# Performance work log

Hardware: AMD Instinct MI355X
Metric: run time of the kernel (lower is better)

## Reference

```python
import jax, jax.numpy as jnp
import numpy as np

# dims
B, S, E, H, W = 32, 256, 512, 512, 512   # batch, max_sentence_length, word_emb, rnn_units, weight_size
ENC = 2 * H                               # bidirectional encoder hidden
V = 50000                                 # vocab


def setup_inputs() -> dict:
    key = jax.random.key(0)
    ks = jax.random.split(key, 16)
    n = jax.random.normal
    return {
        "word_ids": jax.random.randint(ks[0], (B, S), 0, V),
        "encoder_outputs": n(ks[1], (B, S, ENC), jnp.float32),
        "encoder_hn": n(ks[2], (B, H), jnp.float32),          # initial decoder cell state
        "emb": n(ks[3], (V, E), jnp.float32) * 0.02,          # WordFeature embedding table
        "chunk_emb": n(ks[4], (S, W), jnp.float32) * 0.02,    # chunk_length_embedding
        "W1": n(ks[5], (ENC, W), jnp.float32) / np.sqrt(ENC),
        "W2": n(ks[6], (E, W), jnp.float32) / np.sqrt(E),
        "W3": n(ks[7], (E, W), jnp.float32) / np.sqrt(E),
        "W4": n(ks[8], (H, W), jnp.float32) / np.sqrt(H),
        "vt1": n(ks[9], (W,), jnp.float32) / np.sqrt(W),
        "vt2": n(ks[10], (W,), jnp.float32) / np.sqrt(W),
        "Wx": n(ks[11], (E, 4 * H), jnp.float32) / np.sqrt(E),  # decoder LSTM cell
        "Wh": n(ks[12], (H, 4 * H), jnp.float32) / np.sqrt(H),
        "bias": jnp.zeros((4 * H,), jnp.float32),
    }


def reference(word_ids, encoder_outputs, encoder_hn, emb, chunk_emb,
              W1, W2, W3, W4, vt1, vt2, Wx, Wh, bias):
    Ss = word_ids.shape[1]
    Hh = encoder_hn.shape[1]
    inp = emb[word_ids]                                   # [B,S,E] word features
    b1 = jnp.einsum('bse,ew->bsw', encoder_outputs, W1)   # W1(encoder_output), hoisted
    b2 = jnp.einsum('bse,ew->bsw', inp, W2)               # W2(single_input), hoisted
    pos = jnp.arange(Ss)

    def decode_one(inp_b, b1_b, b2_b, c0):
        def step(carry, _):
            last_bond, bond, h, c, out_vec = carry
            done = bond >= Ss
            # decoder input: mean of current segment inp[last_bond:bond] (zeros at step 0)
            m = ((pos >= last_bond) & (pos < bond)).astype(inp_b.dtype)  # [S]
            x = (m @ inp_b) / jnp.maximum(m.sum(), 1.0)                  # [E]
            # LSTM cell (stand-in for decoder.pointer_forward)
            gates = x @ Wx + h @ Wh + bias                               # [4H]
            i_g, f_g, g_g, o_g = jnp.split(gates, 4)
            c_n = jax.nn.sigmoid(f_g) * c + jax.nn.sigmoid(i_g) * jnp.tanh(g_g)
            h_n = jax.nn.sigmoid(o_g) * jnp.tanh(c_n)
            h2 = jnp.where(done, h, h_n)
            c2 = jnp.where(done, c, c_n)
            bidx = jnp.minimum(bond, Ss - 1)
            # pointer attention over positions >= bond
            blend = jnp.tanh(b1_b + b2_b + inp_b[bidx] @ W3 + h2 @ W4)   # [S,W]
            seg_len = jnp.clip(bond - last_bond, 0, Ss - 1)
            scores = blend @ vt1 + chunk_emb[seg_len] @ vt2              # [S]
            scores = jnp.where(pos >= bidx, scores, -1e30)
            # log_softmax is monotonic -> argmax of scores == argmax of log-probs
            idx = jnp.argmax(scores)                                     # absolute = max_index + bond
            new_bond = jnp.where(idx > bond, idx, bond + 1)              # force progress
            widx = jnp.minimum(new_bond, Ss - 1)
            val = jnp.where((~done) & (new_bond < Ss), 1.0, out_vec[widx])
            out_new = out_vec.at[widx].set(val)
            last2 = jnp.where(done, last_bond, bond)
            bond2 = jnp.where(done, bond, new_bond)
            return (last2, bond2, h2, c2, out_new), None

        init = (jnp.int32(0), jnp.int32(0),
                jnp.zeros((Hh,), inp_b.dtype), c0,
                jnp.zeros((Ss,), inp_b.dtype))
        (_, _, _, _, out_vec), _ = jax.lax.scan(step, init, None, length=Ss)
        return out_vec

    outs = jax.vmap(decode_one)(inp, b1, b2, encoder_hn)   # [B,S]
    return outs.T                                          # [S,B] == torch.stack(output_list, 1)
```

## Files before the change

kernel.cpp:

```cpp
#include <hip/hip_runtime.h>
#include <math.h>

#define Bn   32
#define Sn   256
#define En   512
#define Hn   512
#define Wn   512
#define ENCn 1024
#define G4   2048
#define KTOT 1536

#define OFF_BSUM  0L
#define OFF_U3    4194304L
#define OFF_PE    8388608L
#define OFF_WB    12599296L
#define OFF_W4B   14696448L
#define OFF_GATES 14958592L
#define OFF_H     15089664L
#define OFF_C     15106048L
#define OFF_SPART 15138816L
#define OFF_STATE 15204352L

typedef unsigned long long u64t;

__device__ __forceinline__ float aload(const float* p) {
    return __hip_atomic_load(p, __ATOMIC_RELAXED, __HIP_MEMORY_SCOPE_AGENT);
}
__device__ __forceinline__ void astore(float* p, float v) {
    __hip_atomic_store(p, v, __ATOMIC_RELAXED, __HIP_MEMORY_SCOPE_AGENT);
}
__device__ __forceinline__ int aiload(const int* p) {
    return __hip_atomic_load(p, __ATOMIC_RELAXED, __HIP_MEMORY_SCOPE_AGENT);
}
__device__ __forceinline__ void aistore(int* p, int v) {
    __hip_atomic_store(p, v, __ATOMIC_RELAXED, __HIP_MEMORY_SCOPE_AGENT);
}
__device__ __forceinline__ u64t aload64(const u64t* p) {
    return __hip_atomic_load(p, __ATOMIC_RELAXED, __HIP_MEMORY_SCOPE_AGENT);
}
__device__ __forceinline__ void astore64(u64t* p, u64t v) {
    __hip_atomic_store(p, v, __ATOMIC_RELAXED, __HIP_MEMORY_SCOPE_AGENT);
}
__device__ __forceinline__ u64t pack2(float a, float b) {
    return (u64t)__float_as_uint(a) | ((u64t)__float_as_uint(b) << 32);
}
__device__ __forceinline__ float lo32(u64t v) { return __uint_as_float((unsigned)(v & 0xffffffffu)); }
__device__ __forceinline__ float hi32(u64t v) { return __uint_as_float((unsigned)(v >> 32)); }

__global__ void init_kernel(const float* __restrict__ hn0, float* __restrict__ h,
                            float* __restrict__ c, int* __restrict__ state)
{
    int i = blockIdx.x * blockDim.x + threadIdx.x;
    if (i < Bn * Hn) { h[i] = 0.0f; c[i] = hn0[i]; }
    if (i < 8192) state[i] = 0;
}

__global__ void wtrans_kernel(const float* __restrict__ Wx, const float* __restrict__ Wh,
                              const float* __restrict__ W4, float* __restrict__ WB,
                              float* __restrict__ W4B)
{
    int idx = blockIdx.x * 256 + threadIdx.x;
    if (idx < 2097152) {
        const int cc = idx & 3, l = (idx >> 2) & 63, kq = (idx >> 8) & 255, cb = idx >> 16;
        const int k = 4 * kq + cc, j = cb * 64 + l;
        WB[idx] = (k < 512) ? Wx[(long)k * G4 + j] : Wh[(long)(k - 512) * G4 + j];
    }
    if (idx < 262144) {
        const int cc = idx & 3, l = (idx >> 2) & 63, kq = (idx >> 8) & 127, cb = idx >> 15;
        const int k = 4 * kq + cc, j = cb * 64 + l;
        W4B[idx] = W4[(long)k * Wn + j];
    }
}

__global__ void pe1_kernel(const int* __restrict__ wid, const float* __restrict__ emb,
                           float* __restrict__ pb)
{
    const int b = blockIdx.x, blk = blockIdx.y;
    __shared__ int wids[16];
    if (threadIdx.x < 16) wids[threadIdx.x] = wid[b * Sn + blk * 16 + threadIdx.x];
    __syncthreads();
    float a0 = 0.f, a1 = 0.f;
    for (int s = 0; s < 16; ++s) {
        const float* r = emb + (long)wids[s] * En;
        a0 += r[threadIdx.x]; a1 += r[threadIdx.x + 256];
    }
    pb[((long)b * 16 + blk) * En + threadIdx.x] = a0;
    pb[((long)b * 16 + blk) * En + threadIdx.x + 256] = a1;
}

__global__ void pe2_kernel(const int* __restrict__ wid, const float* __restrict__ emb,
                           const float* __restrict__ pb, float* __restrict__ pe)
{
    const int b = blockIdx.x, blk = blockIdx.y;
    __shared__ int wids[16];
    if (threadIdx.x < 16) wids[threadIdx.x] = wid[b * Sn + blk * 16 + threadIdx.x];
    __syncthreads();
    float a0 = 0.f, a1 = 0.f;
    for (int j = 0; j < blk; ++j) {
        a0 += pb[((long)b * 16 + j) * En + threadIdx.x];
        a1 += pb[((long)b * 16 + j) * En + threadIdx.x + 256];
    }
    float* base = pe + (long)b * 257 * En;
    if (blk == 0) { base[threadIdx.x] = 0.f; base[threadIdx.x + 256] = 0.f; }
    for (int s = 0; s < 16; ++s) {
        const float* r = emb + (long)wids[s] * En;
        a0 += r[threadIdx.x]; a1 += r[threadIdx.x + 256];
        float* o = base + (long)(blk * 16 + s + 1) * En;
        o[threadIdx.x] = a0; o[threadIdx.x + 256] = a1;
    }
}

__global__ __launch_bounds__(256) void bsum_gemm(
    const float* __restrict__ enc, const int* __restrict__ wid,
    const float* __restrict__ emb, const float* __restrict__ W1,
    const float* __restrict__ W2, float* __restrict__ bsum)
{
    __shared__ float As[16][68];
    __shared__ float Bs[16][68];
    const int tid  = threadIdx.x;
    const int row0 = blockIdx.y * 64;
    const int col0 = blockIdx.x * 64;
    const int tm0  = (tid & 15) * 4;
    const int tn0  = (tid >> 4) * 4;
    const int la_r = tid >> 2;
    const int la_k = (tid & 3) * 4;
    const int lb_k = tid >> 4;
    const int lb_n = (tid & 15) * 4;

    float acc[4][4];
#pragma unroll
    for (int i = 0; i < 4; i++)
#pragma unroll
        for (int j = 0; j < 4; j++) acc[i][j] = 0.0f;

    for (int k0 = 0; k0 < KTOT; k0 += 16) {
        const int gr = row0 + la_r;
        float4 av;
        if (k0 < ENCn) {
            av = *(const float4*)&enc[(long)gr * ENCn + k0 + la_k];
        } else {
            const int wv = wid[gr];
            av = *(const float4*)&emb[(long)wv * En + (k0 - ENCn) + la_k];
        }
        As[la_k + 0][la_r] = av.x;
        As[la_k + 1][la_r] = av.y;
        As[la_k + 2][la_r] = av.z;
        As[la_k + 3][la_r] = av.w;
        float4 bv;
        if (k0 < ENCn) bv = *(const float4*)&W1[(long)(k0 + lb_k) * Wn + col0 + lb_n];
        else           bv = *(const float4*)&W2[(long)(k0 - ENCn + lb_k) * Wn + col0 + lb_n];
        *(float4*)&Bs[lb_k][lb_n] = bv;
        __syncthreads();
#pragma unroll
        for (int kk = 0; kk < 16; kk++) {
            float4 a = *(const float4*)&As[kk][tm0];
            float4 b = *(const float4*)&Bs[kk][tn0];
            acc[0][0] += a.x * b.x; acc[0][1] += a.x * b.y; acc[0][2] += a.x * b.z; acc[0][3] += a.x * b.w;
            acc[1][0] += a.y * b.x; acc[1][1] += a.y * b.y; acc[1][2] += a.y * b.z; acc[1][3] += a.y * b.w;
            acc[2][0] += a.z * b.x; acc[2][1] += a.z * b.y; acc[2][2] += a.z * b.z; acc[2][3] += a.z * b.w;
            acc[3][0] += a.w * b.x; acc[3][1] += a.w * b.y; acc[3][2] += a.w * b.z; acc[3][3] += a.w * b.w;
        }
        __syncthreads();
    }
#pragma unroll
    for (int i = 0; i < 4; i++) {
        float4 o = make_float4(acc[i][0], acc[i][1], acc[i][2], acc[i][3]);
        *(float4*)&bsum[(long)(row0 + tm0 + i) * Wn + col0 + tn0] = o;
    }
}

__global__ __launch_bounds__(256) void u3_gemm(
    const int* __restrict__ wid, const float* __restrict__ emb,
    const float* __restrict__ W3, float* __restrict__ u3)
{
    __shared__ float As[16][68];
    __shared__ float Bs[16][68];
    const int tid  = threadIdx.x;
    const int row0 = blockIdx.y * 64;
    const int col0 = blockIdx.x * 64;
    const int tm0  = (tid & 15) * 4;
    const int tn0  = (tid >> 4) * 4;
    const int la_r = tid >> 2;
    const int la_k = (tid & 3) * 4;
    const int lb_k = tid >> 4;
    const int lb_n = (tid & 15) * 4;

    float acc[4][4];
#pragma unroll
    for (int i = 0; i < 4; i++)
#pragma unroll
        for (int j = 0; j < 4; j++) acc[i][j] = 0.0f;

    for (int k0 = 0; k0 < 512; k0 += 16) {
        const int gr = row0 + la_r;
        const int wv = wid[gr];
        float4 av = *(const float4*)&emb[(long)wv * En + k0 + la_k];
        As[la_k + 0][la_r] = av.x;
        As[la_k + 1][la_r] = av.y;
        As[la_k + 2][la_r] = av.z;
        As[la_k + 3][la_r] = av.w;
        *(float4*)&Bs[lb_k][lb_n] = *(const float4*)&W3[(long)(k0 + lb_k) * Wn + col0 + lb_n];
        __syncthreads();
#pragma unroll
        for (int kk = 0; kk < 16; kk++) {
            float4 a = *(const float4*)&As[kk][tm0];
            float4 b = *(const float4*)&Bs[kk][tn0];
            acc[0][0] += a.x * b.x; acc[0][1] += a.x * b.y; acc[0][2] += a.x * b.z; acc[0][3] += a.x * b.w;
            acc[1][0] += a.y * b.x; acc[1][1] += a.y * b.y; acc[1][2] += a.y * b.z; acc[1][3] += a.y * b.w;
            acc[2][0] += a.z * b.x; acc[2][1] += a.z * b.y; acc[2][2] += a.z * b.z; acc[2][3] += a.z * b.w;
            acc[3][0] += a.w * b.x; acc[3][1] += a.w * b.y; acc[3][2] += a.w * b.z; acc[3][3] += a.w * b.w;
        }
        __syncthreads();
    }
#pragma unroll
    for (int i = 0; i < 4; i++) {
        float4 o = make_float4(acc[i][0], acc[i][1], acc[i][2], acc[i][3]);
        *(float4*)&u3[(long)(row0 + tm0 + i) * Wn + col0 + tn0] = o;
    }
}

__global__ __launch_bounds__(256) void decode_kernel(
    const float* __restrict__ bias, const float* __restrict__ vt1,
    const float* __restrict__ bsum, const float* __restrict__ u3,
    const float* __restrict__ pe,   const float* __restrict__ WB,
    const float* __restrict__ W4B,  float* __restrict__ gpart,
    float* __restrict__ hbuf, float* __restrict__ cbuf,
    float* __restrict__ spart,
    int* __restrict__ state, float* __restrict__ out)
{
    __shared__ __align__(16) float wlds[32768];
    __shared__ __align__(16) float sx[4096];
    __shared__ __align__(16) float sred[2048];
    __shared__ float s_svt[64];
    __shared__ float s_wv[4];
    __shared__ int   s_wi[4];
    __shared__ int   s_bd[8], s_ls[8];
    __shared__ int   s_exit;

    const int wg   = blockIdx.x;
    const int tid  = threadIdx.x;
    const int lane = tid & 63;
    const int wv   = tid >> 6;

    u64t* s64   = (u64t*)state;
    int*  garr  = state + 2560;
    int*  sflag = state + 4608;

    const int cb1 = wg & 31;
    const int kh  = (wg >> 5) & 1;
    const int bg  = wg >> 6;
    const int b2  = wg >> 3;
    const int cb2 = wg & 7;
    const int bq2 = (wg >> 3) & 7;
    const float4* W4B4 = (const float4*)W4B;
    float4* wlds4 = (float4*)wlds;
    float4* sx4   = (float4*)sx;
    u64t* gp64 = (u64t*)gpart;
    u64t* h64  = (u64t*)hbuf;
    u64t* c64  = (u64t*)cbuf;
    const float2* pef2  = (const float2*)pe;
    const float2* bias2 = (const float2*)bias;

    {
        const float4* src = (const float4*)WB + ((long)cb1 * 256 + kh * 128) * 64;
        for (int i = tid; i < 8192; i += 256) wlds4[i] = src[i];
    }
    if (tid < 64) s_svt[tid] = vt1[cb2 * 64 + tid];

    int a_b = 0;

    for (int t = 1; t <= Sn; ++t) {
        if (tid < 64) {
            const bool isb = tid < 8;
            const u64t* sp = s64 + 768 + 16 * (bg * 8 + (tid & 7));
            for (;;) {
                const u64t pk = isb ? aload64(sp) : 0ULL;
                const int ep = (int)(pk & 0xffffu);
                const int bd = (int)((pk >> 16) & 0xffffu);
                const bool ok = !isb || (ep >= t - 1) || (bd >= Sn);
                const bool dn = isb && (bd >= Sn);
                const u64t okb = __ballot(ok);
                const u64t dnb = __ballot(dn);
                if ((okb & 0xffULL) == 0xffULL) {
                    if (isb) { s_bd[tid] = bd; s_ls[tid] = (int)((pk >> 32) & 0xffffu); }
                    if (tid == 0) s_exit = ((dnb & 0xffULL) == 0xffULL);
                    break;
                }
                __builtin_amdgcn_s_sleep(1);
            }
        }
        __syncthreads();
        if (s_exit) break;

        for (int idx = tid; idx < 2048; idx += 256) {
            const int bq = idx >> 8, kp = idx & 255;
            const int b  = bg * 8 + bq;
            float v0 = 0.f, v1 = 0.f;
            if (s_bd[bq] < Sn) {
                if (kh == 0) {
                    const int bd = s_bd[bq], ls = s_ls[bq];
                    const float inv = 1.0f / (float)max(bd - ls, 1);
                    const float2 pa = pef2[((long)b * 257 + bd) * 256 + kp];
                    const float2 pb_ = pef2[((long)b * 257 + ls) * 256 + kp];
                    v0 = (pa.x - pb_.x) * inv;
                    v1 = (pa.y - pb_.y) * inv;
                } else {
                    const u64t hv = aload64(&h64[b * 256 + kp]);
                    v0 = lo32(hv); v1 = hi32(hv);
                }
            }
            sx[bq * 512 + 2 * kp]     = v0;
            sx[bq * 512 + 2 * kp + 1] = v1;
        }
        __syncthreads();
        {
            float acc[8] = {0.f,0.f,0.f,0.f,0.f,0.f,0.f,0.f};
            const float4* wl = wlds4 + (wv * 32) * 64 + lane;
#pragma unroll 8
            for (int kq = 0; kq < 32; ++kq) {
                const float4 w = wl[kq * 64];
                const int kb = wv * 32 + kq;
#pragma unroll
                for (int bq = 0; bq < 8; ++bq) {
                    const float4 xv = sx4[bq * 128 + kb];
                    acc[bq] += w.x * xv.x + w.y * xv.y + w.z * xv.z + w.w * xv.w;
                }
            }
#pragma unroll
            for (int bq = 0; bq < 8; ++bq)
                sred[wv * 512 + bq * 64 + lane] = acc[bq];
        }
        __syncthreads();
        {
            const int bq = tid >> 5, cp = tid & 31;
            if (s_bd[bq] < Sn) {
                const int c0 = 2 * cp, c1 = 2 * cp + 1;
                const float lo = sred[bq * 64 + c0] + sred[512 + bq * 64 + c0]
                               + sred[1024 + bq * 64 + c0] + sred[1536 + bq * 64 + c0];
                const float hi = sred[bq * 64 + c1] + sred[512 + bq * 64 + c1]
                               + sred[1024 + bq * 64 + c1] + sred[1536 + bq * 64 + c1];
                astore64(&gp64[(long)(kh * Bn + bg * 8 + bq) * 1024 + cb1 * 32 + cp], pack2(lo, hi));
            }
        }
        __syncthreads();
        if (tid < 8)
            aistore(&garr[64 * (bg * 8 + tid) + cb1 * 2 + kh], t);

        const int bd = s_bd[bq2];
        if (bd < Sn) {
            ++a_b;
            if (tid < 64) {
                while (aiload(&garr[64 * b2 + tid]) < t) __builtin_amdgcn_s_sleep(1);
            }
            __syncthreads();
            {
                const long base0 = (long)b2 * 1024;
                const long base1 = (long)(Bn + b2) * 1024;
                const u64t gi0 = aload64(&gp64[base0 + 0 * 256 + tid]);
                const u64t gf0 = aload64(&gp64[base0 + 1 * 256 + tid]);
                const u64t gg0 = aload64(&gp64[base0 + 2 * 256 + tid]);
                const u64t go0 = aload64(&gp64[base0 + 3 * 256 + tid]);
                const u64t gi1 = aload64(&gp64[base1 + 0 * 256 + tid]);
                const u64t gf1 = aload64(&gp64[base1 + 1 * 256 + tid]);
                const u64t gg1 = aload64(&gp64[base1 + 2 * 256 + tid]);
                const u64t go1 = aload64(&gp64[base1 + 3 * 256 + tid]);
                const u64t cv  = aload64(&c64[((a_b - 1) & 1) * 8192 + b2 * 256 + tid]);
                const float2 bi = bias2[0 * 256 + tid];
                const float2 bf = bias2[1 * 256 + tid];
                const float2 bg_ = bias2[2 * 256 + tid];
                const float2 bo = bias2[3 * 256 + tid];
                float h2a, h2b, cna, cnb;
                {
                    const float ig = lo32(gi0) + lo32(gi1) + bi.x;
                    const float fg = lo32(gf0) + lo32(gf1) + bf.x;
                    const float gg = lo32(gg0) + lo32(gg1) + bg_.x;
                    const float og = lo32(go0) + lo32(go1) + bo.x;
                    const float sf = 1.f / (1.f + expf(-fg));
                    const float si = 1.f / (1.f + expf(-ig));
                    const float so = 1.f / (1.f + expf(-og));
                    cna = sf * lo32(cv) + si * tanhf(gg);
                    h2a = so * tanhf(cna);
                }
                {
                    const float ig = hi32(gi0) + hi32(gi1) + bi.y;
                    const float fg = hi32(gf0) + hi32(gf1) + bf.y;
                    const float gg = hi32(gg0) + hi32(gg1) + bg_.y;
                    const float og = hi32(go0) + hi32(go1) + bo.y;
                    const float sf = 1.f / (1.f + expf(-fg));
                    const float si = 1.f / (1.f + expf(-ig));
                    const float so = 1.f / (1.f + expf(-og));
                    cnb = sf * hi32(cv) + si * tanhf(gg);
                    h2b = so * tanhf(cnb);
                }
                sx[2 * tid]     = h2a;
                sx[2 * tid + 1] = h2b;
                if (cb2 == 0) {
                    astore64(&h64[b2 * 256 + tid], pack2(h2a, h2b));
                    astore64(&c64[(a_b & 1) * 8192 + b2 * 256 + tid], pack2(cna, cnb));
                }
            }
            __syncthreads();
            {
                float acc = 0.f;
                const float4* wrow = W4B4 + ((long)cb2 * 128 + wv * 32) * 64 + lane;
#pragma unroll 8
                for (int kq = 0; kq < 32; ++kq) {
                    const float4 w  = wrow[(long)kq * 64];
                    const float4 xv = sx4[wv * 32 + kq];
                    acc += w.x * xv.x + w.y * xv.y + w.z * xv.z + w.w * xv.w;
                }
                sx[512 + wv * 64 + lane] = acc;
            }
            __syncthreads();
            if (tid < 64) {
                const float* u3row = u3 + ((long)b2 * Sn + bd) * Wn + cb2 * 64;
                sx[768 + tid] = sx[512 + tid] + sx[576 + tid] + sx[640 + tid]
                              + sx[704 + tid] + u3row[tid];
            }
            __syncthreads();
            if (tid >= bd) {
                const float* row = bsum + ((long)b2 * Sn + tid) * Wn + cb2 * 64;
                float a = 0.f;
#pragma unroll 8
                for (int i = 0; i < 64; ++i)
                    a += tanhf(row[i] + sx[768 + i]) * s_svt[i];
                astore(&spart[((long)b2 * 8 + cb2) * 256 + tid], a);
            }
            __syncthreads();
            if (cb2 != 0) {
                if (tid == 0) aistore(&sflag[16 * b2 + cb2], a_b);
            } else {
                if (tid >= 1 && tid < 8) {
                    while (aiload(&sflag[16 * b2 + tid]) < a_b) __builtin_amdgcn_s_sleep(1);
                }
                __syncthreads();
                float v = -3.402823e38f; int vi = Sn;
                if (tid >= bd) {
                    const float* sp = spart + (long)b2 * 8 * 256 + tid;
                    float s = 0.f;
#pragma unroll
                    for (int k = 0; k < 8; ++k) s += aload(&sp[k * 256]);
                    v = s; vi = tid;
                }
#pragma unroll
                for (int off = 32; off; off >>= 1) {
                    const float v2 = __shfl_xor(v, off, 64);
                    const int   i2 = __shfl_xor(vi, off, 64);
                    if (v2 > v || (v2 == v && i2 < vi)) { v = v2; vi = i2; }
                }
                if (lane == 0) { s_wv[wv] = v; s_wi[wv] = vi; }
                __syncthreads();
                if (tid == 0) {
                    float bv = s_wv[0]; int bi_ = s_wi[0];
#pragma unroll
                    for (int k = 1; k < 4; ++k)
                        if (s_wv[k] > bv || (s_wv[k] == bv && s_wi[k] < bi_)) { bv = s_wv[k]; bi_ = s_wi[k]; }
                    const int nb2 = (bi_ > bd) ? bi_ : bd + 1;
                    if (nb2 < Sn) out[nb2 * Bn + b2] = 1.0f;
                    const u64t pk =
                        (u64t)(unsigned)t |
                        ((u64t)(unsigned)nb2 << 16) |
                        ((u64t)(unsigned)bd  << 32);
                    astore64(&s64[768 + 16 * b2], pk);
                }
            }
        }
    }
}

extern "C" void kernel_launch(void* const* d_in, const int* in_sizes, int n_in,
                              void* d_out, int out_size, void* d_ws, size_t ws_size,
                              hipStream_t stream)
{
    const int*   wid  = (const int*)d_in[0];
    const float* enc  = (const float*)d_in[1];
    const float* hn0  = (const float*)d_in[2];
    const float* emb  = (const float*)d_in[3];
    const float* W1   = (const float*)d_in[5];
    const float* W2   = (const float*)d_in[6];
    const float* W3   = (const float*)d_in[7];
    const float* W4   = (const float*)d_in[8];
    const float* vt1  = (const float*)d_in[9];
    const float* Wx   = (const float*)d_in[11];
    const float* Wh   = (const float*)d_in[12];
    const float* bias = (const float*)d_in[13];

    float* ws    = (float*)d_ws;
    float* bsum  = ws + OFF_BSUM;
    float* u3    = ws + OFF_U3;
    float* pb    = ws + OFF_U3;
    float* pe    = ws + OFF_PE;
    float* WB    = ws + OFF_WB;
    float* W4B   = ws + OFF_W4B;
    float* gpart = ws + OFF_GATES;
    float* h     = ws + OFF_H;
    float* c     = ws + OFF_C;
    float* spart = ws + OFF_SPART;
    int*   state = (int*)(ws + OFF_STATE);
    float* out   = (float*)d_out;

    hipMemsetAsync(d_out, 0, (size_t)Sn * Bn * sizeof(float), stream);
    hipLaunchKernelGGL(init_kernel, dim3(64), dim3(256), 0, stream, hn0, h, c, state);
    hipLaunchKernelGGL(wtrans_kernel, dim3(8192), dim3(256), 0, stream, Wx, Wh, W4, WB, W4B);
    hipLaunchKernelGGL(pe1_kernel, dim3(32, 16), dim3(256), 0, stream, wid, emb, pb);
    hipLaunchKernelGGL(pe2_kernel, dim3(32, 16), dim3(256), 0, stream, wid, emb, pb, pe);
    hipLaunchKernelGGL(u3_gemm, dim3(8, 128), dim3(256), 0, stream, wid, emb, W3, u3);
    hipLaunchKernelGGL(bsum_gemm, dim3(8, 128), dim3(256), 0, stream, enc, wid, emb, W1, W2, bsum);

    void* args[] = { (void*)&bias, (void*)&vt1, (void*)&bsum, (void*)&u3, (void*)&pe,
                     (void*)&WB, (void*)&W4B, (void*)&gpart, (void*)&h, (void*)&c,
                     (void*)&spart, (void*)&state, (void*)&out };
    hipLaunchCooperativeKernel((void*)decode_kernel, dim3(256), dim3(256), args, 0, stream);
}
```

Baseline: 800.5 us.

## Decouple x and h gate phases with separate flags and redundant per-block argmax

Splits the gate partial buffers into an input part and a double-buffered hidden part. Blocks computing the h-side product now wait only on a per-batch h-ready flag, while x-side blocks wait on the bond state, which loosens the coupling between the two halves. The cross-block argmax reduction is now done redundantly by all eight score blocks, so each keeps its own bond locally instead of waiting on a single leader block. The u3 row is prefetched before the gate wait. In exchange the protocol gains more flags and parity-indexed buffers, which raises the risk of ordering races.

```diff
diff --git a/kernel.cpp b/kernel.cpp
--- a/kernel.cpp
+++ b/kernel.cpp
@@ -9,17 +9,19 @@
 #define ENCn 1024
 #define G4   2048
 #define KTOT 1536
+#define BIGF 0x40000000
 
 #define OFF_BSUM  0L
 #define OFF_U3    4194304L
 #define OFF_PE    8388608L
 #define OFF_WB    12599296L
 #define OFF_W4B   14696448L
-#define OFF_GATES 14958592L
-#define OFF_H     15089664L
-#define OFF_C     15106048L
-#define OFF_SPART 15138816L
-#define OFF_STATE 15204352L
+#define OFF_GPX   14958592L
+#define OFF_GPH   15024128L
+#define OFF_H     15155200L
+#define OFF_C     15171584L
+#define OFF_SPART 15204352L
+#define OFF_STATE 15335424L
 
 typedef unsigned long long u64t;
 
@@ -223,7 +225,8 @@
     const float* __restrict__ bias, const float* __restrict__ vt1,
     const float* __restrict__ bsum, const float* __restrict__ u3,
     const float* __restrict__ pe,   const float* __restrict__ WB,
-    const float* __restrict__ W4B,  float* __restrict__ gpart,
+    const float* __restrict__ W4B,  float* __restrict__ gpx,
+    float* __restrict__ gph,
     float* __restrict__ hbuf, float* __restrict__ cbuf,
     float* __restrict__ spart,
     int* __restrict__ state, float* __restrict__ out)
@@ -235,29 +238,30 @@
     __shared__ float s_wv[4];
     __shared__ int   s_wi[4];
     __shared__ int   s_bd[8], s_ls[8];
-    __shared__ int   s_exit;
+    __shared__ int   s_p1done;
 
     const int wg   = blockIdx.x;
     const int tid  = threadIdx.x;
     const int lane = tid & 63;
     const int wv   = tid >> 6;
 
-    u64t* s64   = (u64t*)state;
-    int*  garr  = state + 2560;
-    int*  sflag = state + 4608;
+    u64t* s64g  = (u64t*)state;
+    int*  hflag = state + 1024;
+    int*  garr  = state + 2048;
+    int*  sflag = state + 4096;
 
     const int cb1 = wg & 31;
     const int kh  = (wg >> 5) & 1;
     const int bg  = wg >> 6;
     const int b2  = wg >> 3;
     const int cb2 = wg & 7;
-    const int bq2 = (wg >> 3) & 7;
     const float4* W4B4 = (const float4*)W4B;
     float4* wlds4 = (float4*)wlds;
     float4* sx4   = (float4*)sx;
-    u64t* gp64 = (u64t*)gpart;
-    u64t* h64  = (u64t*)hbuf;
-    u64t* c64  = (u64t*)cbuf;
+    u64t* gpx64 = (u64t*)gpx;
+    u64t* gph64 = (u64t*)gph;
+    u64t* h64   = (u64t*)hbuf;
+    u64t* c64   = (u64t*)cbuf;
     const float2* pef2  = (const float2*)pe;
     const float2* bias2 = (const float2*)bias;
 
@@ -267,108 +271,137 @@
     }
     if (tid < 64) s_svt[tid] = vt1[cb2 * 64 + tid];
 
-    int a_b = 0;
+    bool p1done = false, p2done = false;
+    int my_bd = 0, my_ls = 0;
 
     for (int t = 1; t <= Sn; ++t) {
-        if (tid < 64) {
-            const bool isb = tid < 8;
-            const u64t* sp = s64 + 768 + 16 * (bg * 8 + (tid & 7));
-            for (;;) {
-                const u64t pk = isb ? aload64(sp) : 0ULL;
-                const int ep = (int)(pk & 0xffffu);
-                const int bd = (int)((pk >> 16) & 0xffffu);
-                const bool ok = !isb || (ep >= t - 1) || (bd >= Sn);
-                const bool dn = isb && (bd >= Sn);
-                const u64t okb = __ballot(ok);
-                const u64t dnb = __ballot(dn);
-                if ((okb & 0xffULL) == 0xffULL) {
-                    if (isb) { s_bd[tid] = bd; s_ls[tid] = (int)((pk >> 32) & 0xffffu); }
-                    if (tid == 0) s_exit = ((dnb & 0xffULL) == 0xffULL);
-                    break;
-                }
-                __builtin_amdgcn_s_sleep(1);
+        if (p1done && p2done) break;
+
+        if (!p1done) {
+            if (kh == 0) {
+                if (tid < 64) {
+                    const bool isb = tid < 8;
+                    const u64t* sp = s64g + 8 * (bg * 8 + (tid & 7));
+                    for (;;) {
+                        const u64t pk = isb ? aload64(sp) : 0ULL;
+                        const int ep = (int)(pk & 0xffffu);
+                        const int bd = (int)((pk >> 16) & 0xffffu);
+                        const bool ok = !isb || (ep >= t - 1) || (bd >= Sn);
+                        const u64t okb = __ballot(ok);
+                        const u64t dnb = __ballot(isb && (bd >= Sn));
+                        if ((okb & 0xffULL) == 0xffULL) {
+                            if (isb) { s_bd[tid] = bd; s_ls[tid] = (int)((pk >> 32) & 0xffffu); }
+                            if (tid == 0) s_p1done = ((dnb & 0xffULL) == 0xffULL);
+                            break;
+                        }
+                        __builtin_amdgcn_s_sleep(1);
+                    }
+                }
+            } else {
+                if (tid < 64) {
+                    const bool isb = tid < 8;
+                    const int* hp = hflag + 16 * (bg * 8 + (tid & 7));
+                    for (;;) {
+                        const int hf = isb ? aiload(hp) : 0x7ffffff0;
+                        const bool ok = (hf >= t - 1);
+                        const u64t okb = __ballot(ok);
+                        const u64t dnb = __ballot(isb && (hf >= BIGF));
+                        if ((okb & 0xffULL) == 0xffULL) {
+                            if (isb) { s_bd[tid] = (hf >= BIGF) ? Sn : 0; s_ls[tid] = 0; }
+                            if (tid == 0) s_p1done = ((dnb & 0xffULL) == 0xffULL);
+                            break;
+                        }
+                        __builtin_amdgcn_s_sleep(1);
+                    }
+                }
+            }
+            __syncthreads();
+            if (s_p1done) p1done = true;
+            if (!p1done) {
+                for (int idx = tid; idx < 2048; idx += 256) {
+                    const int bq = idx >> 8, kp = idx & 255;
+                    const int b  = bg * 8 + bq;
+                    float v0 = 0.f, v1 = 0.f;
+                    if (s_bd[bq] < Sn) {
+                        if (kh == 0) {
+                            const int bd = s_bd[bq], ls = s_ls[bq];
+                            const float inv = 1.0f / (float)max(bd - ls, 1);
+                            const float2 pa  = pef2[((long)b * 257 + bd) * 256 + kp];
+                            const float2 pb_ = pef2[((long)b * 257 + ls) * 256 + kp];
+                            v0 = (pa.x - pb_.x) * inv;
+                            v1 = (pa.y - pb_.y) * inv;
+                        } else {
+                            const u64t hv = aload64(&h64[b * 256 + kp]);
+                            v0 = lo32(hv); v1 = hi32(hv);
+                        }
+                    }
+                    sx[bq * 512 + 2 * kp]     = v0;
+                    sx[bq * 512 + 2 * kp + 1] = v1;
+                }
+                __syncthreads();
+                {
+                    float acc[8] = {0.f,0.f,0.f,0.f,0.f,0.f,0.f,0.f};
+                    const float4* wl = wlds4 + (wv * 32) * 64 + lane;
+#pragma unroll 8
+                    for (int kq = 0; kq < 32; ++kq) {
+                        const float4 w = wl[kq * 64];
+                        const int kb = wv * 32 + kq;
+#pragma unroll
+                        for (int bq = 0; bq < 8; ++bq) {
+                            const float4 xv = sx4[bq * 128 + kb];
+                            acc[bq] += w.x * xv.x + w.y * xv.y + w.z * xv.z + w.w * xv.w;
+                        }
+                    }
+#pragma unroll
+                    for (int bq = 0; bq < 8; ++bq)
+                        sred[wv * 512 + bq * 64 + lane] = acc[bq];
+                }
+                __syncthreads();
+                {
+                    const int bq = tid >> 5, cp = tid & 31;
+                    if (s_bd[bq] < Sn) {
+                        const int c0 = 2 * cp, c1 = 2 * cp + 1;
+                        const float lo = sred[bq * 64 + c0] + sred[512 + bq * 64 + c0]
+                                       + sred[1024 + bq * 64 + c0] + sred[1536 + bq * 64 + c0];
+                        const float hi = sred[bq * 64 + c1] + sred[512 + bq * 64 + c1]
+                                       + sred[1024 + bq * 64 + c1] + sred[1536 + bq * 64 + c1];
+                        if (kh == 0)
+                            astore64(&gpx64[(long)(bg * 8 + bq) * 1024 + cb1 * 32 + cp], pack2(lo, hi));
+                        else
+                            astore64(&gph64[(long)(t & 1) * 32768 + (long)(bg * 8 + bq) * 1024 + cb1 * 32 + cp], pack2(lo, hi));
+                    }
+                }
+                __syncthreads();
+                if (tid < 8)
+                    aistore(&garr[64 * (bg * 8 + tid) + cb1 * 2 + kh], t);
             }
         }
-        __syncthreads();
-        if (s_exit) break;
-
-        for (int idx = tid; idx < 2048; idx += 256) {
-            const int bq = idx >> 8, kp = idx & 255;
-            const int b  = bg * 8 + bq;
-            float v0 = 0.f, v1 = 0.f;
-            if (s_bd[bq] < Sn) {
-                if (kh == 0) {
-                    const int bd = s_bd[bq], ls = s_ls[bq];
-                    const float inv = 1.0f / (float)max(bd - ls, 1);
-                    const float2 pa = pef2[((long)b * 257 + bd) * 256 + kp];
-                    const float2 pb_ = pef2[((long)b * 257 + ls) * 256 + kp];
-                    v0 = (pa.x - pb_.x) * inv;
-                    v1 = (pa.y - pb_.y) * inv;
-                } else {
-                    const u64t hv = aload64(&h64[b * 256 + kp]);
-                    v0 = lo32(hv); v1 = hi32(hv);
-                }
-            }
-            sx[bq * 512 + 2 * kp]     = v0;
-            sx[bq * 512 + 2 * kp + 1] = v1;
-        }
-        __syncthreads();
-        {
-            float acc[8] = {0.f,0.f,0.f,0.f,0.f,0.f,0.f,0.f};
-            const float4* wl = wlds4 + (wv * 32) * 64 + lane;
-#pragma unroll 8
-            for (int kq = 0; kq < 32; ++kq) {
-                const float4 w = wl[kq * 64];
-                const int kb = wv * 32 + kq;
-#pragma unroll
-                for (int bq = 0; bq < 8; ++bq) {
-                    const float4 xv = sx4[bq * 128 + kb];
-                    acc[bq] += w.x * xv.x + w.y * xv.y + w.z * xv.z + w.w * xv.w;
-                }
-            }
-#pragma unroll
-            for (int bq = 0; bq < 8; ++bq)
-                sred[wv * 512 + bq * 64 + lane] = acc[bq];
-        }
-        __syncthreads();
-        {
-            const int bq = tid >> 5, cp = tid & 31;
-            if (s_bd[bq] < Sn) {
-                const int c0 = 2 * cp, c1 = 2 * cp + 1;
-                const float lo = sred[bq * 64 + c0] + sred[512 + bq * 64 + c0]
-                               + sred[1024 + bq * 64 + c0] + sred[1536 + bq * 64 + c0];
-                const float hi = sred[bq * 64 + c1] + sred[512 + bq * 64 + c1]
-                               + sred[1024 + bq * 64 + c1] + sred[1536 + bq * 64 + c1];
-                astore64(&gp64[(long)(kh * Bn + bg * 8 + bq) * 1024 + cb1 * 32 + cp], pack2(lo, hi));
-            }
-        }
-        __syncthreads();
-        if (tid < 8)
-            aistore(&garr[64 * (bg * 8 + tid) + cb1 * 2 + kh], t);
-
-        const int bd = s_bd[bq2];
-        if (bd < Sn) {
-            ++a_b;
+
+        if (!p2done) {
+            const int bd = my_bd;
+            float u3v = 0.f;
+            if (tid < 64) u3v = aload(&u3[((long)b2 * Sn + bd) * Wn + cb2 * 64 + tid]);
             if (tid < 64) {
-                while (aiload(&garr[64 * b2 + tid]) < t) __builtin_amdgcn_s_sleep(1);
+                const int* gp = garr + 64 * b2 + tid;
+                while (aiload(gp) < t) __builtin_amdgcn_s_sleep(1);
             }
             __syncthreads();
             {
-                const long base0 = (long)b2 * 1024;
-                const long base1 = (long)(Bn + b2) * 1024;
-                const u64t gi0 = aload64(&gp64[base0 + 0 * 256 + tid]);
-                const u64t gf0 = aload64(&gp64[base0 + 1 * 256 + tid]);
-                const u64t gg0 = aload64(&gp64[base0 + 2 * 256 + tid]);
-                const u64t go0 = aload64(&gp64[base0 + 3 * 256 + tid]);
-                const u64t gi1 = aload64(&gp64[base1 + 0 * 256 + tid]);
-                const u64t gf1 = aload64(&gp64[base1 + 1 * 256 + tid]);
-                const u64t gg1 = aload64(&gp64[base1 + 2 * 256 + tid]);
-                const u64t go1 = aload64(&gp64[base1 + 3 * 256 + tid]);
-                const u64t cv  = aload64(&c64[((a_b - 1) & 1) * 8192 + b2 * 256 + tid]);
-                const float2 bi = bias2[0 * 256 + tid];
-                const float2 bf = bias2[1 * 256 + tid];
+                const long bx = (long)b2 * 1024;
+                const long bh = (long)(t & 1) * 32768 + (long)b2 * 1024;
+                const u64t gi0 = aload64(&gpx64[bx + 0 * 256 + tid]);
+                const u64t gf0 = aload64(&gpx64[bx + 1 * 256 + tid]);
+                const u64t gg0 = aload64(&gpx64[bx + 2 * 256 + tid]);
+                const u64t go0 = aload64(&gpx64[bx + 3 * 256 + tid]);
+                const u64t gi1 = aload64(&gph64[bh + 0 * 256 + tid]);
+                const u64t gf1 = aload64(&gph64[bh + 1 * 256 + tid]);
+                const u64t gg1 = aload64(&gph64[bh + 2 * 256 + tid]);
+                const u64t go1 = aload64(&gph64[bh + 3 * 256 + tid]);
+                const u64t cv  = aload64(&c64[(long)((t - 1) & 1) * 8192 + b2 * 256 + tid]);
+                const float2 bi  = bias2[0 * 256 + tid];
+                const float2 bf  = bias2[1 * 256 + tid];
                 const float2 bg_ = bias2[2 * 256 + tid];
-                const float2 bo = bias2[3 * 256 + tid];
+                const float2 bo  = bias2[3 * 256 + tid];
                 float h2a, h2b, cna, cnb;
                 {
                     const float ig = lo32(gi0) + lo32(gi1) + bi.x;
@@ -396,10 +429,11 @@
                 sx[2 * tid + 1] = h2b;
                 if (cb2 == 0) {
                     astore64(&h64[b2 * 256 + tid], pack2(h2a, h2b));
-                    astore64(&c64[(a_b & 1) * 8192 + b2 * 256 + tid], pack2(cna, cnb));
-                }
-            }
-            __syncthreads();
+                    astore64(&c64[(long)(t & 1) * 8192 + b2 * 256 + tid], pack2(cna, cnb));
+                }
+            }
+            __syncthreads();
+            if (cb2 == 0 && tid == 0) aistore(&hflag[16 * b2], t);
             {
                 float acc = 0.f;
                 const float4* wrow = W4B4 + ((long)cb2 * 128 + wv * 32) * 64 + lane;
@@ -413,9 +447,8 @@
             }
             __syncthreads();
             if (tid < 64) {
-                const float* u3row = u3 + ((long)b2 * Sn + bd) * Wn + cb2 * 64;
                 sx[768 + tid] = sx[512 + tid] + sx[576 + tid] + sx[640 + tid]
-                              + sx[704 + tid] + u3row[tid];
+                              + sx[704 + tid] + u3v;
             }
             __syncthreads();
             if (tid >= bd) {
@@ -424,46 +457,49 @@
 #pragma unroll 8
                 for (int i = 0; i < 64; ++i)
                     a += tanhf(row[i] + sx[768 + i]) * s_svt[i];
-                astore(&spart[((long)b2 * 8 + cb2) * 256 + tid], a);
-            }
-            __syncthreads();
-            if (cb2 != 0) {
-                if (tid == 0) aistore(&sflag[16 * b2 + cb2], a_b);
-            } else {
-                if (tid >= 1 && tid < 8) {
-                    while (aiload(&sflag[16 * b2 + tid]) < a_b) __builtin_amdgcn_s_sleep(1);
-                }
-                __syncthreads();
-                float v = -3.402823e38f; int vi = Sn;
-                if (tid >= bd) {
-                    const float* sp = spart + (long)b2 * 8 * 256 + tid;
-                    float s = 0.f;
-#pragma unroll
-                    for (int k = 0; k < 8; ++k) s += aload(&sp[k * 256]);
-                    v = s; vi = tid;
-                }
-#pragma unroll
-                for (int off = 32; off; off >>= 1) {
-                    const float v2 = __shfl_xor(v, off, 64);
-                    const int   i2 = __shfl_xor(vi, off, 64);
-                    if (v2 > v || (v2 == v && i2 < vi)) { v = v2; vi = i2; }
-                }
-                if (lane == 0) { s_wv[wv] = v; s_wi[wv] = vi; }
-                __syncthreads();
-                if (tid == 0) {
-                    float bv = s_wv[0]; int bi_ = s_wi[0];
-#pragma unroll
-                    for (int k = 1; k < 4; ++k)
-                        if (s_wv[k] > bv || (s_wv[k] == bv && s_wi[k] < bi_)) { bv = s_wv[k]; bi_ = s_wi[k]; }
-                    const int nb2 = (bi_ > bd) ? bi_ : bd + 1;
+                astore(&spart[(long)(t & 1) * 65536 + (long)b2 * 2048 + cb2 * 256 + tid], a);
+            }
+            __syncthreads();
+            if (tid == 0) aistore(&sflag[16 * b2 + cb2], t);
+            if (tid < 8) {
+                const int* sp = sflag + 16 * b2 + tid;
+                while (aiload(sp) < t) __builtin_amdgcn_s_sleep(1);
+            }
+            __syncthreads();
+            float v = -3.402823e38f; int vi = Sn;
+            if (tid >= bd) {
+                const float* sp = spart + (long)(t & 1) * 65536 + (long)b2 * 2048 + tid;
+                float s = 0.f;
+#pragma unroll
+                for (int k = 0; k < 8; ++k) s += aload(&sp[k * 256]);
+                v = s; vi = tid;
+            }
+#pragma unroll
+            for (int off = 32; off; off >>= 1) {
+                const float v2 = __shfl_xor(v, off, 64);
+                const int   i2 = __shfl_xor(vi, off, 64);
+                if (v2 > v || (v2 == v && i2 < vi)) { v = v2; vi = i2; }
+            }
+            if (lane == 0) { s_wv[wv] = v; s_wi[wv] = vi; }
+            __syncthreads();
+            {
+                float bv = s_wv[0]; int bi_ = s_wi[0];
+#pragma unroll
+                for (int k = 1; k < 4; ++k)
+                    if (s_wv[k] > bv || (s_wv[k] == bv && s_wi[k] < bi_)) { bv = s_wv[k]; bi_ = s_wi[k]; }
+                const int nb2 = (bi_ > bd) ? bi_ : bd + 1;
+                my_ls = bd; my_bd = nb2;
+                if (cb2 == 0 && tid == 0) {
                     if (nb2 < Sn) out[nb2 * Bn + b2] = 1.0f;
-                    const u64t pk =
-                        (u64t)(unsigned)t |
-                        ((u64t)(unsigned)nb2 << 16) |
-                        ((u64t)(unsigned)bd  << 32);
-                    astore64(&s64[768 + 16 * b2], pk);
-                }
-            }
+                    const u64t pk = (u64t)(unsigned)t |
+                                    ((u64t)(unsigned)nb2 << 16) |
+                                    ((u64t)(unsigned)bd  << 32);
+                    astore64(&s64g[8 * b2], pk);
+                    if (nb2 >= Sn) aistore(&hflag[16 * b2], BIGF);
+                }
+                if (nb2 >= Sn) p2done = true;
+            }
+            __syncthreads();
         }
     }
 }
@@ -492,14 +528,15 @@
     float* pe    = ws + OFF_PE;
     float* WB    = ws + OFF_WB;
     float* W4B   = ws + OFF_W4B;
-    float* gpart = ws + OFF_GATES;
+    float* gpx   = ws + OFF_GPX;
+    float* gph   = ws + OFF_GPH;
     float* h     = ws + OFF_H;
     float* c     = ws + OFF_C;
     float* spart = ws + OFF_SPART;
     int*   state = (int*)(ws + OFF_STATE);
     float* out   = (float*)d_out;
 
-    hipMemsetAsync(d_out, 0, (size_t)Sn * Bn * sizeof(float), stream);
+    (void)hipMemsetAsync(d_out, 0, (size_t)Sn * Bn * sizeof(float), stream);
     hipLaunchKernelGGL(init_kernel, dim3(64), dim3(256), 0, stream, hn0, h, c, state);
     hipLaunchKernelGGL(wtrans_kernel, dim3(8192), dim3(256), 0, stream, Wx, Wh, W4, WB, W4B);
     hipLaunchKernelGGL(pe1_kernel, dim3(32, 16), dim3(256), 0, stream, wid, emb, pb);
@@ -508,7 +545,7 @@
     hipLaunchKernelGGL(bsum_gemm, dim3(8, 128), dim3(256), 0, stream, enc, wid, emb, W1, W2, bsum);
 
     void* args[] = { (void*)&bias, (void*)&vt1, (void*)&bsum, (void*)&u3, (void*)&pe,
-                     (void*)&WB, (void*)&W4B, (void*)&gpart, (void*)&h, (void*)&c,
+                     (void*)&WB, (void*)&W4B, (void*)&gpx, (void*)&gph, (void*)&h, (void*)&c,
                      (void*)&spart, (void*)&state, (void*)&out };
-    hipLaunchCooperativeKernel((void*)decode_kernel, dim3(256), dim3(256), args, 0, stream);
-}
+    (void)hipLaunchCooperativeKernel((void*)decode_kernel, dim3(256), dim3(256), args, 0, stream);
+}
```

After: 796.1 us. No clear change (-0.5%).
